# Kernel optimization log

Measured on AMD Instinct MI355X. Metric: run time of the kernel, lower is better.

Reference implementation:

```python
import jax, jax.numpy as jnp
import numpy as np

N_NODES = 100000
N_EDGES = 640000
IN_C, HID_C, OUT_C = 128, 256, 128
N_GRAPHS = 64


def setup_inputs() -> dict:
    key = jax.random.key(0)
    k1, k2, k3, k4, k5, k6, k7 = jax.random.split(key, 7)
    x = jax.random.normal(k1, (N_NODES, IN_C), dtype=jnp.float32)
    edge_index = jax.random.randint(k2, (2, N_EDGES), 0, N_NODES, dtype=jnp.int32)
    batch = jnp.sort(jax.random.randint(k3, (N_NODES,), 0, N_GRAPHS, dtype=jnp.int32))
    s1 = 1.0 / np.sqrt(IN_C)
    s2 = 1.0 / np.sqrt(HID_C)
    W1 = jax.random.uniform(k4, (IN_C, HID_C), jnp.float32, -s1, s1)
    b1 = jax.random.uniform(k5, (HID_C,), jnp.float32, -s1, s1)
    W2 = jax.random.uniform(k6, (HID_C, OUT_C), jnp.float32, -s2, s2)
    b2 = jax.random.uniform(k7, (OUT_C,), jnp.float32, -s2, s2)
    return {"x": x, "edge_index": edge_index, "batch": batch,
            "W1": W1, "b1": b1, "W2": W2, "b2": b2}


def gcn_conv(x, src, dst, W, b, n_nodes):
    # GCNConv: D^{-1/2} (A + I) D^{-1/2} X W + b, degrees computed with self-loops
    ones = jnp.ones(src.shape[0], dtype=x.dtype)
    deg = jax.ops.segment_sum(ones, dst, num_segments=n_nodes) + 1.0  # self-loop
    inv_sqrt_deg = jax.lax.rsqrt(deg)
    h = x @ W  # [N, out]
    coef = inv_sqrt_deg[src] * inv_sqrt_deg[dst]  # [E]
    msgs = h[src] * coef[:, None]  # [E, out] -- dominant memory traffic
    agg = jax.ops.segment_sum(msgs, dst, num_segments=n_nodes)
    agg = agg + h * (inv_sqrt_deg * inv_sqrt_deg)[:, None]  # self-loop term
    return agg + b


def reference(x, edge_index, batch, W1, b1, W2, b2):
    n = x.shape[0]
    src, dst = edge_index[0], edge_index[1]
    h = jax.nn.relu(gcn_conv(x, src, dst, W1, b1, n))
    h = jax.nn.relu(gcn_conv(h, src, dst, W2, b2, n))
    # global mean pool over graphs
    sums = jax.ops.segment_sum(h, batch, num_segments=N_GRAPHS)
    counts = jax.ops.segment_sum(jnp.ones(n, dtype=h.dtype), batch, num_segments=N_GRAPHS)
    graph_embed = sums / jnp.maximum(counts, 1.0)[:, None]
    return h, graph_embed
```

## Files before the change

### kernel.cpp

```cpp
#include <hip/hip_runtime.h>

#define N_NODES  100000
#define N_EDGES  640000
#define IN_C     128
#define HID_C    256
#define OUT_C    128
#define N_GRAPHS 64
#define CAP      32

#define NBUK     256
#define NPB      ((N_NODES + NBUK - 1) / NBUK)
#define NSTRIPE  8
#define SCAP     448
#define BPB      (NSTRIPE * SCAP)
#define EPB      4096
#define EBLK     ((N_EDGES + EPB - 1) / EPB)

typedef _Float16 f16;
typedef _Float16 f16x8 __attribute__((ext_vector_type(8)));
typedef float    f32x4 __attribute__((ext_vector_type(4)));


__global__ void zero_gcur_kernel(int* __restrict__ g) {
    int i = blockIdx.x * 256 + threadIdx.x;
    if (i < NBUK * NSTRIPE) g[i] = 0;
}


__global__ __launch_bounds__(256) void phaseA_kernel(
    const int* __restrict__ src, const int* __restrict__ dst,
    int* __restrict__ gcur, int* __restrict__ buckets,
    const float* __restrict__ x, f16* __restrict__ xh,
    const float* __restrict__ W1, f16* __restrict__ Wt1,
    const float* __restrict__ W2, f16* __restrict__ Wt2,
    int* __restrict__ gs) {
    int b = blockIdx.x;
    if (b < EBLK) {
        __shared__ int bcnt[NBUK];
        __shared__ int bbase[NBUK];
        int tid = threadIdx.x;
        int st  = b & (NSTRIPE - 1);
        for (int i = tid; i < NBUK; i += 256) bcnt[i] = 0;
        __syncthreads();
        int e0 = b * EPB + tid * 16;
        bool act = e0 < N_EDGES;
        int bk[16], pp[16], val[16];
        #pragma unroll
        for (int c = 0; c < 4; ++c) {
            int e = e0 + c * 4;
            int4 dq = act ? *reinterpret_cast<const int4*>(&dst[e]) : make_int4(0,0,0,0);
            int4 sq = act ? *reinterpret_cast<const int4*>(&src[e]) : make_int4(0,0,0,0);
            int dv[4] = {dq.x, dq.y, dq.z, dq.w};
            int sv[4] = {sq.x, sq.y, sq.z, sq.w};
            #pragma unroll
            for (int j = 0; j < 4; ++j) {
                int k = c * 4 + j;
                int bkj = (unsigned)dv[j] / NPB;
                bk[k]  = bkj;
                val[k] = ((dv[j] - bkj * NPB) << 17) | sv[j];
            }
        }
        #pragma unroll
        for (int k = 0; k < 16; ++k)
            pp[k] = act ? atomicAdd(&bcnt[bk[k]], 1) : 0;
        __syncthreads();
        if (tid < NBUK) {
            int c = bcnt[tid];
            if (c > 0) bbase[tid] = atomicAdd(&gcur[tid * NSTRIPE + st], c);
        }
        __syncthreads();
        if (act) {
            #pragma unroll
            for (int k = 0; k < 16; ++k) {
                int idx = bbase[bk[k]] + pp[k];
                if (idx < SCAP)
                    buckets[(size_t)bk[k] * BPB + st * SCAP + idx] = val[k];
            }
        }
        return;
    }
    b -= EBLK;
    if (b < 6250) {
        int i = (b * 256 + threadIdx.x) * 8;
        float4 a = *reinterpret_cast<const float4*>(&x[i]);
        float4 c = *reinterpret_cast<const float4*>(&x[i + 4]);
        f16x8 o = { (f16)a.x, (f16)a.y, (f16)a.z, (f16)a.w,
                    (f16)c.x, (f16)c.y, (f16)c.z, (f16)c.w };
        *reinterpret_cast<f16x8*>(&xh[i]) = o;
        return;
    }
    b -= 6250;
    if (b < 128) {
        int idx = b * 256 + threadIdx.x;
        int k = idx / HID_C, n = idx % HID_C;
        Wt1[n * IN_C + k] = (f16)W1[idx];
        return;
    }
    b -= 128;
    if (b < 128) {
        int idx = b * 256 + threadIdx.x;
        int k = idx / OUT_C, n = idx % OUT_C;
        Wt2[n * HID_C + k] = (f16)W2[idx];
        return;
    }
    if (threadIdx.x <= N_GRAPHS) gs[threadIdx.x] = N_NODES;
}
#define PHASEA_BLOCKS (EBLK + 6250 + 128 + 128 + 1)


__global__ __launch_bounds__(256) void phaseB_kernel(
    const int* __restrict__ gcur, const int* __restrict__ buckets,
    int2* __restrict__ meta, int* __restrict__ slots, float* __restrict__ isd,
    const int* __restrict__ batch, int* __restrict__ gs) {
    int b = blockIdx.x;
    if (b < NBUK) {
        __shared__ int cur[NPB];
        int tid = threadIdx.x;
        int v0 = b * NPB;
        int nv = min(NPB, N_NODES - v0);
        for (int i = tid; i < NPB; i += 256) cur[i] = 0;
        __syncthreads();
        for (int s = 0; s < NSTRIPE; ++s) {
            int n = min(gcur[b * NSTRIPE + s], SCAP);
            const int* seg = &buckets[(size_t)b * BPB + s * SCAP];
            for (int i = tid; i < n; i += 256) {
                int e = seg[i];
                int r = e >> 17;
                int pos = atomicAdd(&cur[r], 1);
                if (pos < CAP) slots[(size_t)(v0 + r) * CAP + pos] = e & 0x1FFFF;
            }
        }
        __syncthreads();
        for (int i = tid; i < nv; i += 256) {
            int c = cur[i];
            float iv = rsqrtf((float)c + 1.0f);
            meta[v0 + i] = make_int2(c, __float_as_int(iv));
            isd[v0 + i] = iv;
        }
        return;
    }
    b -= NBUK;
    int i = b * 256 + threadIdx.x;
    if (i < N_NODES) {
        int bt = batch[i];
        int pb = (i == 0) ? -1 : batch[i - 1];
        for (int g = pb + 1; g <= bt; ++g) gs[g] = i;
    }
}
#define PHASEB_BLOCKS (NBUK + (N_NODES + 255) / 256)


template <int N, int K, int NBLK, bool BIAS_RELU, bool SCALE>
__global__ __launch_bounds__(256) void gemm_lds_kernel(
    const f16* __restrict__ A, const f16* __restrict__ Wt,
    const float* __restrict__ bias, const float* __restrict__ isd,
    f16* __restrict__ Cmat, int M) {
    constexpr int KS = K / 32;
    constexpr int NT = NBLK / 16;
    constexpr int KP = K + 8;
    __shared__ f16 Bs[NBLK * KP];

    int tid  = threadIdx.x;
    int wid  = tid >> 6;
    int lane = tid & 63;
    int l16  = lane & 15;
    int kgrp = lane >> 4;
    int rowbase = blockIdx.x * 128 + wid * 32;
    int col0    = blockIdx.y * NBLK;

    constexpr int CH = NBLK * K / 8;
    #pragma unroll
    for (int c = tid; c < CH; c += 256) {
        int row = c / (K / 8);
        int c8  = c % (K / 8);
        *reinterpret_cast<f16x8*>(&Bs[row * KP + c8 * 8]) =
            *reinterpret_cast<const f16x8*>(&Wt[(size_t)(col0 + row) * K + c8 * 8]);
    }

    f16x8 a[2][KS];
    f16x8 zero = {};
    #pragma unroll
    for (int rt = 0; rt < 2; ++rt) {
        int r = rowbase + rt * 16 + l16;
        bool ok = r < M;
        #pragma unroll
        for (int s = 0; s < KS; ++s)
            a[rt][s] = ok ? *reinterpret_cast<const f16x8*>(
                                &A[(size_t)r * K + s * 32 + kgrp * 8])
                          : zero;
    }
    __syncthreads();

    f32x4 acc[2][NT] = {};
    #pragma unroll
    for (int c = 0; c < NT; ++c) {
        #pragma unroll
        for (int s = 0; s < KS; ++s) {
            f16x8 b = *reinterpret_cast<const f16x8*>(
                &Bs[(c * 16 + l16) * KP + s * 32 + kgrp * 8]);
            acc[0][c] = __builtin_amdgcn_mfma_f32_16x16x32_f16(a[0][s], b, acc[0][c], 0, 0, 0);
            acc[1][c] = __builtin_amdgcn_mfma_f32_16x16x32_f16(a[1][s], b, acc[1][c], 0, 0, 0);
        }
    }

    #pragma unroll
    for (int c = 0; c < NT; ++c) {
        int col = col0 + c * 16 + l16;
        float bv = BIAS_RELU ? bias[col] : 0.f;
        #pragma unroll
        for (int rt = 0; rt < 2; ++rt) {
            int crow0 = rowbase + rt * 16 + kgrp * 4;
            #pragma unroll
            for (int j = 0; j < 4; ++j) {
                int row = crow0 + j;
                if (row < M) {
                    float v = acc[rt][c][j];
                    if constexpr (BIAS_RELU) v = fmaxf(v + bv, 0.f);
                    if constexpr (SCALE)     v *= isd[row];
                    Cmat[(size_t)row * N + col] = (f16)v;
                }
            }
        }
    }
}


template <bool COEF, bool BIAS_RELU, typename OutT>
__global__ __launch_bounds__(256) void agg_kernel(
    const f16* __restrict__ h, const int2* __restrict__ meta,
    const int* __restrict__ slots, const float* __restrict__ bias,
    OutT* __restrict__ out) {
    constexpr int C = 128;
    int wid  = threadIdx.x >> 6;
    int lane = threadIdx.x & 63;
    int q    = lane >> 4;
    int ln   = lane & 15;
    int vA = blockIdx.x * 8 + wid * 2;
    if (vA >= N_NODES) return;
    int vB = vA + 1;
    bool hasB = vB < N_NODES;
    int baseA = vA * CAP;
    int baseB = hasB ? vB * CAP : 0;

    int2 mA = meta[vA];
    int2 mB = hasB ? meta[vB] : make_int2(0, 0);
    int ra0 = slots[baseA + q];
    int ra1 = slots[baseA + q + 4];
    int rb0 = slots[baseB + q];
    int rb1 = slots[baseB + q + 4];
    f16x8 hvS = {};
    if (q < 2 && (q == 0 || hasB)) {
        int vS = q ? vB : vA;
        hvS = *reinterpret_cast<const f16x8*>(&h[(size_t)vS * C + ln * 8]);
    }

    int ia0 = ((unsigned)ra0 < N_NODES) ? ra0 : 0;
    int ia1 = ((unsigned)ra1 < N_NODES) ? ra1 : 0;
    int ib0 = ((unsigned)rb0 < N_NODES) ? rb0 : 0;
    int ib1 = ((unsigned)rb1 < N_NODES) ? rb1 : 0;

    f16x8 ha0 = *reinterpret_cast<const f16x8*>(&h[(size_t)ia0 * C + ln * 8]);
    f16x8 ha1 = *reinterpret_cast<const f16x8*>(&h[(size_t)ia1 * C + ln * 8]);
    f16x8 hb0 = *reinterpret_cast<const f16x8*>(&h[(size_t)ib0 * C + ln * 8]);
    f16x8 hb1 = *reinterpret_cast<const f16x8*>(&h[(size_t)ib1 * C + ln * 8]);

    int eA = min(mA.x, CAP);
    int eB = hasB ? min(mB.x, CAP) : 0;
    float ivA = __int_as_float(mA.y);
    float ivB = hasB ? __int_as_float(mB.y) : 0.f;

    bool mA0 = q < eA,     mA1 = q + 4 < eA;
    bool mB0 = q < eB,     mB1 = q + 4 < eB;
    f16 ca0, ca1, cb0, cb1;
    if constexpr (COEF) {
        ca0 = (f16)(mA0 ? __int_as_float(meta[ia0].y) * ivA : 0.f);
        ca1 = (f16)(mA1 ? __int_as_float(meta[ia1].y) * ivA : 0.f);
        cb0 = (f16)(mB0 ? __int_as_float(meta[ib0].y) * ivB : 0.f);
        cb1 = (f16)(mB1 ? __int_as_float(meta[ib1].y) * ivB : 0.f);
    } else {
        ca0 = (f16)(mA0 ? 1.f : 0.f);
        ca1 = (f16)(mA1 ? 1.f : 0.f);
        cb0 = (f16)(mB0 ? 1.f : 0.f);
        cb1 = (f16)(mB1 ? 1.f : 0.f);
    }
    f16x8 acc0 = {}, acc1 = {};
    {
        f16x8 va0 = {ca0, ca0, ca0, ca0, ca0, ca0, ca0, ca0};
        f16x8 va1 = {ca1, ca1, ca1, ca1, ca1, ca1, ca1, ca1};
        f16x8 vb0 = {cb0, cb0, cb0, cb0, cb0, cb0, cb0, cb0};
        f16x8 vb1 = {cb1, cb1, cb1, cb1, cb1, cb1, cb1, cb1};
        acc0 += va0 * ha0;
        acc0 += va1 * ha1;
        acc1 += vb0 * hb0;
        acc1 += vb1 * hb1;
    }

    int tA = 8 + q, tB = 8 + q;
    while (__any((tA < eA) || (tB < eB))) {
        bool nA0 = tA < eA, nA1 = tA + 4 < eA;
        bool nB0 = tB < eB, nB1 = tB + 4 < eB;
        int ja0 = slots[baseA + (nA0 ? tA     : 0)];
        int ja1 = slots[baseA + (nA1 ? tA + 4 : 0)];
        int jb0 = slots[baseB + (nB0 ? tB     : 0)];
        int jb1 = slots[baseB + (nB1 ? tB + 4 : 0)];
        ja0 = ((unsigned)ja0 < N_NODES) ? ja0 : 0;
        ja1 = ((unsigned)ja1 < N_NODES) ? ja1 : 0;
        jb0 = ((unsigned)jb0 < N_NODES) ? jb0 : 0;
        jb1 = ((unsigned)jb1 < N_NODES) ? jb1 : 0;
        f16 da0, da1, db0, db1;
        if constexpr (COEF) {
            da0 = (f16)(nA0 ? __int_as_float(meta[ja0].y) * ivA : 0.f);
            da1 = (f16)(nA1 ? __int_as_float(meta[ja1].y) * ivA : 0.f);
            db0 = (f16)(nB0 ? __int_as_float(meta[jb0].y) * ivB : 0.f);
            db1 = (f16)(nB1 ? __int_as_float(meta[jb1].y) * ivB : 0.f);
        } else {
            da0 = (f16)(nA0 ? 1.f : 0.f);
            da1 = (f16)(nA1 ? 1.f : 0.f);
            db0 = (f16)(nB0 ? 1.f : 0.f);
            db1 = (f16)(nB1 ? 1.f : 0.f);
        }
        f16x8 ga0 = *reinterpret_cast<const f16x8*>(&h[(size_t)ja0 * C + ln * 8]);
        f16x8 ga1 = *reinterpret_cast<const f16x8*>(&h[(size_t)ja1 * C + ln * 8]);
        f16x8 gb0 = *reinterpret_cast<const f16x8*>(&h[(size_t)jb0 * C + ln * 8]);
        f16x8 gb1 = *reinterpret_cast<const f16x8*>(&h[(size_t)jb1 * C + ln * 8]);
        f16x8 wa0 = {da0, da0, da0, da0, da0, da0, da0, da0};
        f16x8 wa1 = {da1, da1, da1, da1, da1, da1, da1, da1};
        f16x8 wb0 = {db0, db0, db0, db0, db0, db0, db0, db0};
        f16x8 wb1 = {db1, db1, db1, db1, db1, db1, db1, db1};
        acc0 += wa0 * ga0;
        acc0 += wa1 * ga1;
        acc1 += wb0 * gb0;
        acc1 += wb1 * gb1;
        tA += 8; tB += 8;
    }

    #pragma unroll
    for (int st = 16; st <= 32; st <<= 1) {
        int4 r0 = __builtin_bit_cast(int4, acc0);
        int4 r1 = __builtin_bit_cast(int4, acc1);
        int4 s0, s1;
        s0.x = __shfl_xor(r0.x, st, 64); s0.y = __shfl_xor(r0.y, st, 64);
        s0.z = __shfl_xor(r0.z, st, 64); s0.w = __shfl_xor(r0.w, st, 64);
        s1.x = __shfl_xor(r1.x, st, 64); s1.y = __shfl_xor(r1.y, st, 64);
        s1.z = __shfl_xor(r1.z, st, 64); s1.w = __shfl_xor(r1.w, st, 64);
        acc0 += __builtin_bit_cast(f16x8, s0);
        acc1 += __builtin_bit_cast(f16x8, s1);
    }
    if (q < 2) {
        bool ok = (q == 0) || hasB;
        if (ok) {
            int v = q ? vB : vA;
            float iv = q ? ivB : ivA;
            f16x8 accv = q ? acc1 : acc0;
            float t[8];
            if constexpr (COEF) {
                float cs = iv * iv;
                #pragma unroll
                for (int i = 0; i < 8; ++i) t[i] = (float)accv[i] + cs * (float)hvS[i];
            } else {
                #pragma unroll
                for (int i = 0; i < 8; ++i) t[i] = iv * ((float)accv[i] + (float)hvS[i]);
            }
            if constexpr (BIAS_RELU) {
                float4 b0 = *reinterpret_cast<const float4*>(&bias[ln * 8]);
                float4 b1 = *reinterpret_cast<const float4*>(&bias[ln * 8 + 4]);
                float bb[8] = {b0.x, b0.y, b0.z, b0.w, b1.x, b1.y, b1.z, b1.w};
                float o[8];
                #pragma unroll
                for (int i = 0; i < 8; ++i)
                    o[i] = fmaxf(t[i] + bb[i], 0.f);
                *reinterpret_cast<float4*>(&out[(size_t)v * C + ln * 8]) =
                    make_float4(o[0], o[1], o[2], o[3]);
                *reinterpret_cast<float4*>(&out[(size_t)v * C + ln * 8 + 4]) =
                    make_float4(o[4], o[5], o[6], o[7]);
            } else {
                f16x8 o;
                #pragma unroll
                for (int i = 0; i < 8; ++i) o[i] = (f16)t[i];
                *reinterpret_cast<f16x8*>(&out[(size_t)v * C + ln * 8]) = o;
            }
        }
    }
}


#define POOL_PARTS 16
__global__ void pool_partial_kernel(const float* __restrict__ h, const int* __restrict__ gs,
                                    float* __restrict__ psums) {
    int g    = blockIdx.x >> 4;
    int part = blockIdx.x & 15;
    int ch   = threadIdx.x;
    int s = gs[g], e = gs[g + 1];
    float acc = 0.f;
    for (int i = s + part; i < e; i += POOL_PARTS)
        acc += h[(size_t)i * OUT_C + ch];
    psums[(size_t)(g * POOL_PARTS + part) * OUT_C + ch] = acc;
}

__global__ void pool_final_kernel(const float* __restrict__ psums, const int* __restrict__ gs,
                                  float* __restrict__ out2) {
    int g = blockIdx.x, ch = threadIdx.x;
    float acc = 0.f;
    #pragma unroll
    for (int p = 0; p < POOL_PARTS; ++p)
        acc += psums[(size_t)(g * POOL_PARTS + p) * OUT_C + ch];
    int c = gs[g + 1] - gs[g];
    out2[g * OUT_C + ch] = acc / fmaxf((float)c, 1.0f);
}


extern "C" void kernel_launch(void* const* d_in, const int* in_sizes, int n_in,
                              void* d_out, int out_size, void* d_ws, size_t ws_size,
                              hipStream_t stream) {
    const float* x     = (const float*)d_in[0];
    const int*   ei    = (const int*)d_in[1];
    const int*   src   = ei;
    const int*   dst   = ei + N_EDGES;
    const int*   batch = (const int*)d_in[2];
    const float* W1    = (const float*)d_in[3];
    const float* b1    = (const float*)d_in[4];
    const float* W2    = (const float*)d_in[5];
    const float* b2    = (const float*)d_in[6];

    float* out    = (float*)d_out;
    float* h_out  = out;
    float* ge_out = out + (size_t)N_NODES * OUT_C;

    char* wsp = (char*)d_ws;
    auto alloc = [&](size_t bytes) -> char* {
        char* p = wsp;
        wsp += (bytes + 255) & ~(size_t)255;
        return p;
    };
    int2*  meta    = (int2*)alloc((size_t)N_NODES * 8);
    float* isd     = (float*)alloc((size_t)N_NODES * 4);
    int*   slots   = (int*)alloc((size_t)N_NODES * CAP * 4);
    int*   gcur    = (int*)alloc((size_t)NBUK * NSTRIPE * 4);
    int*   buckets = (int*)alloc((size_t)NBUK * BPB * 4);
    int*   gs      = (int*)alloc((size_t)(N_GRAPHS + 1) * 4);
    float* psums   = (float*)alloc((size_t)N_GRAPHS * POOL_PARTS * OUT_C * 4);
    f16*   xh      = (f16*)alloc((size_t)N_NODES * IN_C * 2);
    f16*   ax      = (f16*)alloc((size_t)N_NODES * IN_C * 2);
    f16*   t1      = (f16*)alloc((size_t)N_NODES * HID_C * 2);
    f16*   t2      = (f16*)alloc((size_t)N_NODES * OUT_C * 2);
    f16*   Wt1     = (f16*)alloc((size_t)IN_C * HID_C * 2);
    f16*   Wt2     = (f16*)alloc((size_t)HID_C * OUT_C * 2);

    zero_gcur_kernel<<<(NBUK * NSTRIPE + 255) / 256, 256, 0, stream>>>(gcur);

    phaseA_kernel<<<PHASEA_BLOCKS, 256, 0, stream>>>(src, dst, gcur, buckets, x, xh,
                                                     W1, Wt1, W2, Wt2, gs);
    phaseB_kernel<<<PHASEB_BLOCKS, 256, 0, stream>>>(gcur, buckets, meta, slots, isd,
                                                     batch, gs);

    agg_kernel<true, false, f16><<<(N_NODES + 7) / 8, 256, 0, stream>>>(
        xh, meta, slots, nullptr, ax);
    {
        dim3 g((N_NODES + 127) / 128, HID_C / 128);
        gemm_lds_kernel<HID_C, IN_C, 128, true, false><<<g, 256, 0, stream>>>(
            ax, Wt1, b1, nullptr, t1, N_NODES);
    }

    {
        dim3 g((N_NODES + 127) / 128, OUT_C / 64);
        gemm_lds_kernel<OUT_C, HID_C, 64, false, true><<<g, 256, 0, stream>>>(
            t1, Wt2, nullptr, isd, t2, N_NODES);
    }
    agg_kernel<false, true, float><<<(N_NODES + 7) / 8, 256, 0, stream>>>(
        t2, meta, slots, b2, h_out);

    pool_partial_kernel<<<N_GRAPHS * POOL_PARTS, OUT_C, 0, stream>>>(h_out, gs, psums);
    pool_final_kernel<<<N_GRAPHS, OUT_C, 0, stream>>>(psums, gs, ge_out);
}
```

Before: 202.8 us.

## Fuse layer-1 and layer-2 GEMMs to keep hidden activations on chip

The two separate GEMM kernels become one fused kernel. Each wave computes a 16-row tile of relu(A·W1+b1) in registers, then transposes it through a small LDS bounce buffer into the A-operand layout and multiplies by W2 straight away. This removes the write and re-read of the 100000x256 f16 hidden tensor t1 and one kernel launch. In exchange, each block reloads both weight matrices into LDS for only 64 rows, which cuts reuse per block. The kernel also holds 16 accumulator tiles in registers, which can lower occupancy.

```diff
diff --git a/kernel.cpp b/kernel.cpp
--- a/kernel.cpp
+++ b/kernel.cpp
@@ -17,6 +17,7 @@
 #define EBLK     ((N_EDGES + EPB - 1) / EPB)
 
 typedef _Float16 f16;
+typedef _Float16 f16x4 __attribute__((ext_vector_type(4)));
 typedef _Float16 f16x8 __attribute__((ext_vector_type(8)));
 typedef float    f32x4 __attribute__((ext_vector_type(4)));
 
@@ -150,77 +151,110 @@
 #define PHASEB_BLOCKS (NBUK + (N_NODES + 255) / 256)
 
 
-template <int N, int K, int NBLK, bool BIAS_RELU, bool SCALE>
-__global__ __launch_bounds__(256) void gemm_lds_kernel(
-    const f16* __restrict__ A, const f16* __restrict__ Wt,
-    const float* __restrict__ bias, const float* __restrict__ isd,
-    f16* __restrict__ Cmat, int M) {
-    constexpr int KS = K / 32;
-    constexpr int NT = NBLK / 16;
-    constexpr int KP = K + 8;
-    __shared__ f16 Bs[NBLK * KP];
-
+__global__ __launch_bounds__(256) void gemm_fused_kernel(
+    const f16* __restrict__ A,
+    const f16* __restrict__ Wt1,
+    const f16* __restrict__ Wt2,
+    const float* __restrict__ b1,
+    const float* __restrict__ isd,
+    f16* __restrict__ T2, int M) {
+    __shared__ f16 Wl[128 * 132];
+    __shared__ f16 bounce[4][2][16 * 40];
     int tid  = threadIdx.x;
     int wid  = tid >> 6;
     int lane = tid & 63;
     int l16  = lane & 15;
     int kgrp = lane >> 4;
-    int rowbase = blockIdx.x * 128 + wid * 32;
-    int col0    = blockIdx.y * NBLK;
-
-    constexpr int CH = NBLK * K / 8;
-    #pragma unroll
-    for (int c = tid; c < CH; c += 256) {
-        int row = c / (K / 8);
-        int c8  = c % (K / 8);
-        *reinterpret_cast<f16x8*>(&Bs[row * KP + c8 * 8]) =
-            *reinterpret_cast<const f16x8*>(&Wt[(size_t)(col0 + row) * K + c8 * 8]);
-    }
-
-    f16x8 a[2][KS];
+    int rowbase = blockIdx.x * 64 + wid * 16;
+    int arow = rowbase + l16;
+    bool okrow = arow < M;
+
+    f16x8 a1[4];
     f16x8 zero = {};
     #pragma unroll
-    for (int rt = 0; rt < 2; ++rt) {
-        int r = rowbase + rt * 16 + l16;
-        bool ok = r < M;
-        #pragma unroll
-        for (int s = 0; s < KS; ++s)
-            a[rt][s] = ok ? *reinterpret_cast<const f16x8*>(
-                                &A[(size_t)r * K + s * 32 + kgrp * 8])
-                          : zero;
-    }
-    __syncthreads();
-
-    f32x4 acc[2][NT] = {};
-    #pragma unroll
-    for (int c = 0; c < NT; ++c) {
-        #pragma unroll
-        for (int s = 0; s < KS; ++s) {
-            f16x8 b = *reinterpret_cast<const f16x8*>(
-                &Bs[(c * 16 + l16) * KP + s * 32 + kgrp * 8]);
-            acc[0][c] = __builtin_amdgcn_mfma_f32_16x16x32_f16(a[0][s], b, acc[0][c], 0, 0, 0);
-            acc[1][c] = __builtin_amdgcn_mfma_f32_16x16x32_f16(a[1][s], b, acc[1][c], 0, 0, 0);
-        }
-    }
-
-    #pragma unroll
-    for (int c = 0; c < NT; ++c) {
-        int col = col0 + c * 16 + l16;
-        float bv = BIAS_RELU ? bias[col] : 0.f;
-        #pragma unroll
-        for (int rt = 0; rt < 2; ++rt) {
-            int crow0 = rowbase + rt * 16 + kgrp * 4;
+    for (int s = 0; s < 4; ++s)
+        a1[s] = okrow ? *reinterpret_cast<const f16x8*>(&A[(size_t)arow * IN_C + s * 32 + kgrp * 8])
+                      : zero;
+
+    f32x4 acc1[16] = {};
+    #pragma unroll
+    for (int c = 0; c < 2; ++c) {
+        #pragma unroll
+        for (int g = 0; g < 8; ++g) {
+            int idx = g * 256 + tid;
+            int col = idx >> 4;
+            int gg  = idx & 15;
+            *reinterpret_cast<f16x8*>(&Wl[col * 132 + gg * 8]) =
+                *reinterpret_cast<const f16x8*>(&Wt1[(size_t)(c * 128 + col) * IN_C + gg * 8]);
+        }
+        __syncthreads();
+        #pragma unroll
+        for (int t = 0; t < 8; ++t) {
+            #pragma unroll
+            for (int s = 0; s < 4; ++s) {
+                f16x8 b = *reinterpret_cast<const f16x8*>(
+                    &Wl[(t * 16 + l16) * 132 + s * 32 + kgrp * 8]);
+                acc1[c * 8 + t] = __builtin_amdgcn_mfma_f32_16x16x32_f16(
+                    a1[s], b, acc1[c * 8 + t], 0, 0, 0);
+            }
+        }
+        __syncthreads();
+    }
+    f16x4 p1[16];
+    #pragma unroll
+    for (int t = 0; t < 16; ++t) {
+        float bb = b1[t * 16 + l16];
+        #pragma unroll
+        for (int j = 0; j < 4; ++j)
+            p1[t][j] = (f16)fmaxf(acc1[t][j] + bb, 0.f);
+    }
+    int crow0 = rowbase + kgrp * 4;
+    float sv[4];
+    #pragma unroll
+    for (int j = 0; j < 4; ++j)
+        sv[j] = (crow0 + j < M) ? isd[crow0 + j] : 0.f;
+
+    #pragma unroll
+    for (int c2 = 0; c2 < 2; ++c2) {
+        #pragma unroll
+        for (int g = 0; g < 8; ++g) {
+            int idx = g * 256 + tid;
+            int col = idx >> 5;
+            int gg  = idx & 31;
+            *reinterpret_cast<f16x8*>(&Wl[col * 260 + gg * 8]) =
+                *reinterpret_cast<const f16x8*>(&Wt2[(size_t)(c2 * 64 + col) * HID_C + gg * 8]);
+        }
+        __syncthreads();
+        f32x4 acc2[4] = {};
+        #pragma unroll
+        for (int s = 0; s < 8; ++s) {
+            f16* buf = &bounce[wid][s & 1][0];
+            #pragma unroll
+            for (int half = 0; half < 2; ++half) {
+                int t = 2 * s + half;
+                #pragma unroll
+                for (int j = 0; j < 4; ++j)
+                    buf[(kgrp * 4 + j) * 40 + half * 16 + l16] = p1[t][j];
+            }
+            f16x8 a2 = *reinterpret_cast<const f16x8*>(&buf[l16 * 40 + kgrp * 8]);
+            #pragma unroll
+            for (int ct = 0; ct < 4; ++ct) {
+                f16x8 b = *reinterpret_cast<const f16x8*>(
+                    &Wl[(ct * 16 + l16) * 260 + s * 32 + kgrp * 8]);
+                acc2[ct] = __builtin_amdgcn_mfma_f32_16x16x32_f16(a2, b, acc2[ct], 0, 0, 0);
+            }
+        }
+        #pragma unroll
+        for (int ct = 0; ct < 4; ++ct) {
+            int col = c2 * 64 + ct * 16 + l16;
             #pragma unroll
             for (int j = 0; j < 4; ++j) {
                 int row = crow0 + j;
-                if (row < M) {
-                    float v = acc[rt][c][j];
-                    if constexpr (BIAS_RELU) v = fmaxf(v + bv, 0.f);
-                    if constexpr (SCALE)     v *= isd[row];
-                    Cmat[(size_t)row * N + col] = (f16)v;
-                }
-            }
-        }
+                if (row < M)
+                    T2[(size_t)row * OUT_C + col] = (f16)(acc2[ct][j] * sv[j]);
+            }
+        }
+        __syncthreads();
     }
 }
 
@@ -441,7 +475,6 @@
     float* psums   = (float*)alloc((size_t)N_GRAPHS * POOL_PARTS * OUT_C * 4);
     f16*   xh      = (f16*)alloc((size_t)N_NODES * IN_C * 2);
     f16*   ax      = (f16*)alloc((size_t)N_NODES * IN_C * 2);
-    f16*   t1      = (f16*)alloc((size_t)N_NODES * HID_C * 2);
     f16*   t2      = (f16*)alloc((size_t)N_NODES * OUT_C * 2);
     f16*   Wt1     = (f16*)alloc((size_t)IN_C * HID_C * 2);
     f16*   Wt2     = (f16*)alloc((size_t)HID_C * OUT_C * 2);
@@ -455,17 +488,10 @@
 
     agg_kernel<true, false, f16><<<(N_NODES + 7) / 8, 256, 0, stream>>>(
         xh, meta, slots, nullptr, ax);
-    {
-        dim3 g((N_NODES + 127) / 128, HID_C / 128);
-        gemm_lds_kernel<HID_C, IN_C, 128, true, false><<<g, 256, 0, stream>>>(
-            ax, Wt1, b1, nullptr, t1, N_NODES);
-    }
-
-    {
-        dim3 g((N_NODES + 127) / 128, OUT_C / 64);
-        gemm_lds_kernel<OUT_C, HID_C, 64, false, true><<<g, 256, 0, stream>>>(
-            t1, Wt2, nullptr, isd, t2, N_NODES);
-    }
+
+    gemm_fused_kernel<<<(N_NODES + 63) / 64, 256, 0, stream>>>(
+        ax, Wt1, Wt2, b1, isd, t2, N_NODES);
+
     agg_kernel<false, true, float><<<(N_NODES + 7) / 8, 256, 0, stream>>>(
         t2, meta, slots, b2, h_out);
 
```

Measured after the change: 181.5 us. -10.5%, faster.
